# Performance work log

Measured on AMD Instinct MI355X. Metric: run time of the kernel, lower is better.

Reference implementation:

```python
import jax, jax.numpy as jnp
import numpy as np

# TT config (matches init_kwargs)
NUM_TABLES = 4
P = (100, 100, 100)          # tt_p_shapes, prod = num_embeddings = 1e6
Q = (4, 4, 4)                # tt_q_shapes, prod = embedding_dim = 64
R = (1, 32, 32, 1)           # tt_ranks with boundary ranks
BAGS_PER_TABLE = 8192
POOL = 16                    # indices per bag


def setup_inputs() -> dict:
    key = jax.random.key(0)
    k1, k2, k3, k4 = jax.random.split(key, 4)
    nnz = NUM_TABLES * BAGS_PER_TABLE * POOL      # 524288
    B = NUM_TABLES * BAGS_PER_TABLE               # 32768 bags total
    indices = jax.random.randint(k1, (nnz,), 0, P[0] * P[1] * P[2], dtype=jnp.int64)
    offsets = (jnp.arange(B + 1, dtype=jnp.int64) * POOL)
    scale = 0.05  # small init, akin to approx-normal weight_dist
    tt_core_0 = jax.random.normal(k2, (NUM_TABLES, P[0], R[0] * Q[0] * R[1]), dtype=jnp.float32) * scale
    tt_core_1 = jax.random.normal(k3, (NUM_TABLES, P[1], R[1] * Q[1] * R[2]), dtype=jnp.float32) * scale
    tt_core_2 = jax.random.normal(k4, (NUM_TABLES, P[2], R[2] * Q[2] * R[3]), dtype=jnp.float32) * scale
    return {"indices": indices, "offsets": offsets,
            "tt_core_0": tt_core_0, "tt_core_1": tt_core_1, "tt_core_2": tt_core_2}


def reference(indices, offsets, tt_core_0, tt_core_1, tt_core_2):
    nnz = indices.shape[0]
    B = offsets.shape[0] - 1
    bags_per_table = B // NUM_TABLES

    # bag id for each nonzero (embedding-bag semantics), then table id per nonzero
    rowidx = jnp.searchsorted(offsets, jnp.arange(nnz, dtype=offsets.dtype), side='right') - 1
    tableidx = rowidx // bags_per_table

    # decompose flat row index into TT indices (C-order over p-shapes,
    # matching tt_matrix_to_full row layout)
    i0 = indices // (P[1] * P[2])
    i1 = (indices // P[2]) % P[1]
    i2 = indices % P[2]

    # gather per-lookup core slices
    c0 = tt_core_0[tableidx, i0].reshape(nnz, Q[0], R[1])          # r0 == 1
    c1 = tt_core_1[tableidx, i1].reshape(nnz, R[1], Q[1], R[2])
    c2 = tt_core_2[tableidx, i2].reshape(nnz, R[2], Q[2])          # r3 == 1

    # on-the-fly TT contraction to reconstruct embedding rows [nnz, D]
    t = jnp.einsum('nar,nrbs->nabs', c0, c1)                       # [nnz, q0, q1, r2]
    rows = jnp.einsum('nabs,nsc->nabc', t, c2).reshape(nnz, Q[0] * Q[1] * Q[2])

    # sum-pool per bag
    out = jax.ops.segment_sum(rows, rowidx, num_segments=B)        # [B, D]
    return out
```

## Files before the change

kernel.cpp:

```cpp
#include <hip/hip_runtime.h>
#include <stdint.h>

#define NT 4
#define PP 100
#define TT_BYTES (4ull * 100 * 100 * 1024)
#define C2B_DWORDS (NT * PP * 64)


typedef short bf16x8 __attribute__((ext_vector_type(8)));
typedef float f32x4  __attribute__((ext_vector_type(4)));
typedef float f32x2  __attribute__((ext_vector_type(2)));

__device__ __forceinline__ uint32_t f2bf(float f) {
    union { float f; uint32_t u; } v; v.f = f;
    uint32_t u = v.u;
    return (u + 0x7fffu + ((u >> 16) & 1u)) >> 16;
}

__global__ __launch_bounds__(256)
void c2pack_kernel(const float* __restrict__ c2g, uint32_t* __restrict__ c2p) {
    int t = blockIdx.x * 256 + threadIdx.x;
    if (t >= C2B_DWORDS) return;
    int sg = t & 15, c = (t >> 4) & 3, combo = t >> 6;
    const float* src = c2g + (size_t)combo * 128;
    c2p[t] = f2bf(src[(2 * sg) * 4 + c]) | (f2bf(src[(2 * sg + 1) * 4 + c]) << 16);
}

__global__ __launch_bounds__(128, 3)
void tt_phase1(const float* __restrict__ c0g, const float* __restrict__ c1g,
               unsigned short* __restrict__ tT) {
    __shared__ float c1s[32 * 128];
    __shared__ float c0t[16 * 132];

    int blk = blockIdx.x;
    int tab   = blk / 700;
    int rem   = blk % 700;
    int i1    = rem / 7;
    int chunk = rem % 7;
    int i0_base = chunk * 16;
    int tid = threadIdx.x;

    const float4* c1p = (const float4*)(c1g + (size_t)(tab * PP + i1) * 4096);
    float4* c1v = (float4*)c1s;
    #pragma unroll
    for (int it = 0; it < 8; ++it) c1v[tid + 128 * it] = c1p[tid + 128 * it];

    #pragma unroll
    for (int it = 0; it < 16; ++it) {
        int f = tid + 128 * it;
        int i0l = f >> 7;
        int x   = f & 127;
        int a = x >> 5, r = x & 31;
        int i0 = i0_base + i0l; if (i0 > PP - 1) i0 = PP - 1;
        c0t[i0l * 132 + r * 4 + a] = c0g[(size_t)(tab * PP + i0) * 128 + x];
    }
    __syncthreads();

    int u  = tid >> 4;
    int sg = tid & 15;

    f32x2 acc[2][16];
    #pragma unroll
    for (int ii = 0; ii < 2; ++ii)
        #pragma unroll
        for (int q = 0; q < 16; ++q) acc[ii][q] = (f32x2){0.f, 0.f};

    #pragma unroll 4
    for (int r = 0; r < 32; ++r) {
        float4 av0 = *(const float4*)&c0t[(2 * u) * 132 + r * 4];
        float4 av1 = *(const float4*)&c0t[(2 * u + 1) * 132 + r * 4];
        const float* a0 = (const float*)&av0;
        const float* a1 = (const float*)&av1;
        #pragma unroll
        for (int b = 0; b < 4; ++b) {
            f32x2 bv = *(const f32x2*)&c1s[r * 128 + b * 32 + 2 * sg];
            #pragma unroll
            for (int a = 0; a < 4; ++a) {
                acc[0][a * 4 + b] += (f32x2){a0[a], a0[a]} * bv;
                acc[1][a * 4 + b] += (f32x2){a1[a], a1[a]} * bv;
            }
        }
    }

    #pragma unroll
    for (int ii = 0; ii < 2; ++ii) {
        int i0 = i0_base + 2 * u + ii;
        if (i0 >= PP) continue;
        size_t combo = (size_t)tab * 10000 + (size_t)i0 * 100 + (size_t)i1;
        char* base = (char*)tT + combo * 1024 + (size_t)sg * 4;
        #pragma unroll
        for (int ab = 0; ab < 16; ++ab) {
            uint32_t w = f2bf(acc[ii][ab].x) | (f2bf(acc[ii][ab].y) << 16);
            *(uint32_t*)(base + ab * 64) = w;
        }
    }
}

__global__ __launch_bounds__(256, 6)
void tt_phase2(const int* __restrict__ indices, const int* __restrict__ offsets,
               const char* __restrict__ tT, const char* __restrict__ c2b,
               float* __restrict__ out, int bags_per_table, int B) {
    __shared__ float red[4][64];
    int lane = threadIdx.x & 63;
    int wv   = threadIdx.x >> 6;
    int bag  = blockIdx.x;
    int col = lane & 15;
    int kq  = lane >> 4;
    int tab = bag / bags_per_table;
    int start = offsets[bag];

    uint32_t idx = (uint32_t)indices[start + wv * 4 + (col & 3)];
    uint32_t i0 = idx / 10000u;
    uint32_t r1 = idx - i0 * 10000u;
    uint32_t i1 = r1 / 100u;
    uint32_t i2 = r1 - i1 * 100u;
    uint32_t tby = (((uint32_t)tab * 10000u + i0 * 100u + i1) << 10);
    uint32_t cby = (((uint32_t)tab * 100u + i2) << 8);

    int aoff = col * 64 + kq * 16;
    int boff = (col & 3) * 64 + kq * 16;

    bf16x8 A[4], Bv[4];
    #pragma unroll
    for (int jj = 0; jj < 4; ++jj) {
        uint32_t tb = (uint32_t)__builtin_amdgcn_readlane((int)tby, jj);
        uint32_t cb = (uint32_t)__builtin_amdgcn_readlane((int)cby, jj);
        A[jj]  = *(const bf16x8*)(tT  + tb + aoff);
        Bv[jj] = *(const bf16x8*)(c2b + cb + boff);
    }

    f32x4 acc = {0.f, 0.f, 0.f, 0.f};
    #pragma unroll
    for (int jj = 0; jj < 4; ++jj)
        acc = __builtin_amdgcn_mfma_f32_16x16x32_bf16(A[jj], Bv[jj], acc, 0, 0, 0);

    if (col < 4) {
        #pragma unroll
        for (int q = 0; q < 4; ++q)
            red[wv][kq * 16 + q * 4 + col] = acc[q];
    }
    __syncthreads();
    if (wv == 0) {
        float s = red[0][lane] + red[1][lane] + red[2][lane] + red[3][lane];
        out[(size_t)bag * 64 + lane] = s;
    }
}

extern "C" void kernel_launch(void* const* d_in, const int* in_sizes, int n_in,
                              void* d_out, int out_size, void* d_ws, size_t ws_size,
                              hipStream_t stream) {
    const int*   indices = (const int*)d_in[0];
    const int*   offsets = (const int*)d_in[1];
    const float* c0      = (const float*)d_in[2];
    const float* c1      = (const float*)d_in[3];
    const float* c2      = (const float*)d_in[4];
    float* out = (float*)d_out;

    int B = in_sizes[1] - 1;
    int bags_per_table = B / NT;

    unsigned short* tT  = (unsigned short*)d_ws;
    uint32_t*       c2p = (uint32_t*)((char*)d_ws + TT_BYTES);

    c2pack_kernel<<<dim3((C2B_DWORDS + 255) / 256), dim3(256), 0, stream>>>(c2, c2p);
    tt_phase1<<<dim3(NT * PP * 7), dim3(128), 0, stream>>>(c0, c1, tT);
    tt_phase2<<<dim3(B), dim3(256), 0, stream>>>(indices, offsets,
                                                 (const char*)tT,
                                                 (const char*)c2p, out,
                                                 bags_per_table, B);
}
```

Before: 154.2 us.

## Use bf16 MFMA for TT phase1 contraction and fuse c2 packing

```diff
diff --git a/kernel.cpp b/kernel.cpp
--- a/kernel.cpp
+++ b/kernel.cpp
@@ -9,7 +9,6 @@
 
 typedef short bf16x8 __attribute__((ext_vector_type(8)));
 typedef float f32x4  __attribute__((ext_vector_type(4)));
-typedef float f32x2  __attribute__((ext_vector_type(2)));
 
 __device__ __forceinline__ uint32_t f2bf(float f) {
     union { float f; uint32_t u; } v; v.f = f;
@@ -18,80 +17,89 @@
 }
 
 __global__ __launch_bounds__(256)
-void c2pack_kernel(const float* __restrict__ c2g, uint32_t* __restrict__ c2p) {
-    int t = blockIdx.x * 256 + threadIdx.x;
-    if (t >= C2B_DWORDS) return;
-    int sg = t & 15, c = (t >> 4) & 3, combo = t >> 6;
-    const float* src = c2g + (size_t)combo * 128;
-    c2p[t] = f2bf(src[(2 * sg) * 4 + c]) | (f2bf(src[(2 * sg + 1) * 4 + c]) << 16);
-}
-
-__global__ __launch_bounds__(128, 3)
 void tt_phase1(const float* __restrict__ c0g, const float* __restrict__ c1g,
-               unsigned short* __restrict__ tT) {
-    __shared__ float c1s[32 * 128];
-    __shared__ float c0t[16 * 132];
+               unsigned short* __restrict__ tT,
+               const float* __restrict__ c2g, uint32_t* __restrict__ c2p) {
+    __shared__ uint32_t       A_l[112 * 16];
+    __shared__ uint32_t       B_l[128 * 16];
+    __shared__ unsigned short D_l[100 * 128];
 
     int blk = blockIdx.x;
-    int tab   = blk / 700;
-    int rem   = blk % 700;
-    int i1    = rem / 7;
-    int chunk = rem % 7;
-    int i0_base = chunk * 16;
     int tid = threadIdx.x;
 
-    const float4* c1p = (const float4*)(c1g + (size_t)(tab * PP + i1) * 4096);
-    float4* c1v = (float4*)c1s;
+    if (blk >= 1600) {
+        int t = (blk - 1600) * 256 + tid;
+        if (t < C2B_DWORDS) {
+            int sg = t & 15, c = (t >> 4) & 3, combo = t >> 6;
+            const float* src = c2g + (size_t)combo * 128;
+            c2p[t] = f2bf(src[(2 * sg) * 4 + c]) | (f2bf(src[(2 * sg + 1) * 4 + c]) << 16);
+        }
+        return;
+    }
+
+    int tab = blk / 400;
+    int rem = blk % 400;
+    int i1  = rem >> 2;
+    int ch  = rem & 3;
+
+    if (tid < 192) A_l[1600 + tid] = 0u;
+
+    const float2* a2 = (const float2*)(c0g + (size_t)tab * 12800 + (size_t)ch * 3200);
     #pragma unroll
-    for (int it = 0; it < 8; ++it) c1v[tid + 128 * it] = c1p[tid + 128 * it];
-
+    for (int it = 0; it < 7; ++it) {
+        int d = tid + it * 256;
+        if (d < 1600) {
+            float2 v = a2[d];
+            int row = d >> 4, kd = d & 15;
+            A_l[row * 16 + (kd ^ ((row & 3) << 2))] = f2bf(v.x) | (f2bf(v.y) << 16);
+        }
+    }
+    const float* c1row = c1g + ((size_t)tab * PP + i1) * 4096;
     #pragma unroll
-    for (int it = 0; it < 16; ++it) {
-        int f = tid + 128 * it;
-        int i0l = f >> 7;
-        int x   = f & 127;
-        int a = x >> 5, r = x & 31;
-        int i0 = i0_base + i0l; if (i0 > PP - 1) i0 = PP - 1;
-        c0t[i0l * 132 + r * 4 + a] = c0g[(size_t)(tab * PP + i0) * 128 + x];
+    for (int it = 0; it < 8; ++it) {
+        int j = tid + it * 256;
+        int n = j & 127, rp = j >> 7;
+        float e = c1row[(2 * rp) * 128 + n];
+        float o = c1row[(2 * rp + 1) * 128 + n];
+        B_l[n * 16 + (rp ^ ((n & 3) << 2))] = f2bf(e) | (f2bf(o) << 16);
     }
     __syncthreads();
 
-    int u  = tid >> 4;
-    int sg = tid & 15;
+    int lane = tid & 63, wv = tid >> 6;
+    int col = lane & 15, kq = lane >> 4;
 
-    f32x2 acc[2][16];
     #pragma unroll
-    for (int ii = 0; ii < 2; ++ii)
+    for (int mt = 0; mt < 7; ++mt) {
         #pragma unroll
-        for (int q = 0; q < 16; ++q) acc[ii][q] = (f32x2){0.f, 0.f};
-
-    #pragma unroll 4
-    for (int r = 0; r < 32; ++r) {
-        float4 av0 = *(const float4*)&c0t[(2 * u) * 132 + r * 4];
-        float4 av1 = *(const float4*)&c0t[(2 * u + 1) * 132 + r * 4];
-        const float* a0 = (const float*)&av0;
-        const float* a1 = (const float*)&av1;
-        #pragma unroll
-        for (int b = 0; b < 4; ++b) {
-            f32x2 bv = *(const f32x2*)&c1s[r * 128 + b * 32 + 2 * sg];
+        for (int ntl = 0; ntl < 2; ++ntl) {
+            int nt = wv * 2 + ntl;
+            int arow = mt * 16 + col;
+            int bn   = nt * 16 + col;
+            bf16x8 af = *(const bf16x8*)&A_l[arow * 16 + ((kq ^ (arow & 3)) << 2)];
+            bf16x8 bf = *(const bf16x8*)&B_l[bn   * 16 + ((kq ^ (bn   & 3)) << 2)];
+            f32x4 acc = {0.f, 0.f, 0.f, 0.f};
+            acc = __builtin_amdgcn_mfma_f32_16x16x32_bf16(af, bf, acc, 0, 0, 0);
             #pragma unroll
-            for (int a = 0; a < 4; ++a) {
-                acc[0][a * 4 + b] += (f32x2){a0[a], a0[a]} * bv;
-                acc[1][a * 4 + b] += (f32x2){a1[a], a1[a]} * bv;
+            for (int q = 0; q < 4; ++q) {
+                int Drow = mt * 16 + kq * 4 + q;
+                if (Drow < 100)
+                    D_l[Drow * 128 + nt * 16 + col] = (unsigned short)f2bf(acc[q]);
             }
         }
     }
+    __syncthreads();
 
     #pragma unroll
-    for (int ii = 0; ii < 2; ++ii) {
-        int i0 = i0_base + 2 * u + ii;
-        if (i0 >= PP) continue;
-        size_t combo = (size_t)tab * 10000 + (size_t)i0 * 100 + (size_t)i1;
-        char* base = (char*)tT + combo * 1024 + (size_t)sg * 4;
-        #pragma unroll
-        for (int ab = 0; ab < 16; ++ab) {
-            uint32_t w = f2bf(acc[ii][ab].x) | (f2bf(acc[ii][ab].y) << 16);
-            *(uint32_t*)(base + ab * 64) = w;
+    for (int it = 0; it < 7; ++it) {
+        int c = tid + it * 256;
+        if (c < 1600) {
+            int Drow = c >> 4, w = c & 15;
+            int i0l = Drow >> 2, a = Drow & 3;
+            int b = w >> 2, so = w & 3;
+            int i0 = ch * 25 + i0l;
+            size_t combo = (size_t)tab * 10000 + (size_t)i0 * 100 + (size_t)i1;
+            char* dst = (char*)tT + combo * 1024 + (size_t)(a * 4 + b) * 64 + (size_t)so * 16;
+            *(uint4*)dst = *(const uint4*)&D_l[Drow * 128 + w * 8];
         }
     }
 }
@@ -162,8 +170,7 @@
     unsigned short* tT  = (unsigned short*)d_ws;
     uint32_t*       c2p = (uint32_t*)((char*)d_ws + TT_BYTES);
 
-    c2pack_kernel<<<dim3((C2B_DWORDS + 255) / 256), dim3(256), 0, stream>>>(c2, c2p);
-    tt_phase1<<<dim3(NT * PP * 7), dim3(128), 0, stream>>>(c0, c1, tT);
+    tt_phase1<<<dim3(1700), dim3(256), 0, stream>>>(c0, c1, tT, c2, c2p);
     tt_phase2<<<dim3(B), dim3(256), 0, stream>>>(indices, offsets,
                                                  (const char*)tT,
                                                  (const char*)c2p, out,
```

After: 144.2 us. -6.5%, faster.
